# Performance work log

Measured on AMD Instinct MI355X. Metric: run time of the kernel, lower is better.

Reference implementation:

```python
import jax, jax.numpy as jnp
import numpy as np

B, N = 8192, 64
EPS = 1e-3  # diagonal jitter to guarantee strict positive-definiteness


def setup_inputs() -> dict:
    key = jax.random.key(0)
    A = jax.random.normal(key, (B, N, N), dtype=jnp.float32)
    # SPD construction: X = A A^T / N + eps*I  (eigenvalues strictly > 0)
    X = jnp.einsum('bik,bjk->bij', A, A) / N + EPS * jnp.eye(N, dtype=jnp.float32)
    return {"X": X}


def reference(X):
    # sym_logm: eig-based matrix logarithm of batched SPD matrices
    w, v = jnp.linalg.eigh(X)                    # w: [B,N], v: [B,N,N]
    logm = jnp.einsum('bik,bk,bjk->bij', v, jnp.log(w), v)  # V diag(log w) V^T
    # embed with tril=False: flatten from dim 1 -> [B, N*N]
    return logm.reshape(logm.shape[0], -1)
```

## Files before the change

### kernel.cpp

```cpp
#include <hip/hip_runtime.h>
#include <math.h>

#define NSW 12

__device__ __forceinline__ float bperm_f(int addr4, float v) {
    return __int_as_float(__builtin_amdgcn_ds_bpermute(addr4, __float_as_int(v)));
}

__global__ __launch_bounds__(128, 4) void logeig_kernel(
    const float* __restrict__ Xg, float* __restrict__ out)
{
    __shared__ __align__(16) float Wc[64 * 20];
    __shared__ float gbuf[2][2][64];
    __shared__ float nbuf[2][64];
    __shared__ float hlds[64];

    const int tid = threadIdx.x;
    const int w   = tid >> 6;
    const int l   = tid & 63;
    const int b   = blockIdx.x;

    float x[32];
    {
        const float4* __restrict__ Xb4 =
            (const float4*)(Xg + (size_t)b * 4096 + (size_t)l * 64 + 32 * w);
        #pragma unroll
        for (int q = 0; q < 8; ++q) {
            float4 v = Xb4[q];
            x[4 * q + 0] = v.x; x[4 * q + 1] = v.y;
            x[4 * q + 2] = v.z; x[4 * q + 3] = v.w;
        }
    }

    float d;
    {
        float a0 = 0.f, a1 = 0.f, a2 = 0.f, a3 = 0.f;
        #pragma unroll
        for (int k = 0; k < 32; k += 4) {
            a0 = fmaf(x[k + 0], x[k + 0], a0);
            a1 = fmaf(x[k + 1], x[k + 1], a1);
            a2 = fmaf(x[k + 2], x[k + 2], a2);
            a3 = fmaf(x[k + 3], x[k + 3], a3);
        }
        nbuf[w][l] = (a0 + a1) + (a2 + a3);
        __syncthreads();
        d = nbuf[0][l] + nbuf[1][l];
    }

    const int m  = l - 1;
    int pm = (l == 0) ? 0 : ((63 - m) % 63);
    int p0 = 0;

    for (int sweep = 0; sweep < NSW; ++sweep) {
        for (int r = 0; r < 63; ++r) {
            const int prt  = (l == 0) ? (p0 + 1)
                                      : ((pm == m) ? 0 : (pm + 1));
            const int prt4 = prt << 2;

            float xp[32];
            float a0 = 0.f, a1 = 0.f, a2 = 0.f, a3 = 0.f;
            #pragma unroll
            for (int k = 0; k < 32; k += 4) {
                xp[k + 0] = bperm_f(prt4, x[k + 0]);
                xp[k + 1] = bperm_f(prt4, x[k + 1]);
                xp[k + 2] = bperm_f(prt4, x[k + 2]);
                xp[k + 3] = bperm_f(prt4, x[k + 3]);
                a0 = fmaf(x[k + 0], xp[k + 0], a0);
                a1 = fmaf(x[k + 1], xp[k + 1], a1);
                a2 = fmaf(x[k + 2], xp[k + 2], a2);
                a3 = fmaf(x[k + 3], xp[k + 3], a3);
            }
            const float gp = (a0 + a1) + (a2 + a3);
            const float dq = bperm_f(prt4, d);

            gbuf[r & 1][w][l] = gp;
            __syncthreads();
            const float go = gbuf[r & 1][1 - w][l];
            const float g  = gp + go;

            const bool lo = l < prt;
            const bool ok = fabsf(g) > 1e-30f;

            const float num  = lo ? (dq - d) : (d - dq);
            const float zeta = num / (2.f * g);
            const float az   = fabsf(zeta);
            float tl = 1.f / (az + sqrtf(fmaf(az, az, 1.f)));
            tl = (zeta >= 0.f) ? tl : -tl;
            float tn = lo ? tl : -tl;
            tn = ok ? tn : 0.f;
            const float c = rsqrtf(fmaf(tn, tn, 1.f));
            const float s = c * tn;

            d = fmaf(-tn, g, d);

            #pragma unroll
            for (int k = 0; k < 32; ++k)
                x[k] = fmaf(-s, xp[k], c * x[k]);

            pm = (pm + 1 == 63) ? 0 : (pm + 1);
            p0 += 32; if (p0 >= 63) p0 -= 63;
        }

        float a0 = 0.f, a1 = 0.f, a2 = 0.f, a3 = 0.f;
        #pragma unroll
        for (int k = 0; k < 32; k += 4) {
            a0 = fmaf(x[k + 0], x[k + 0], a0);
            a1 = fmaf(x[k + 1], x[k + 1], a1);
            a2 = fmaf(x[k + 2], x[k + 2], a2);
            a3 = fmaf(x[k + 3], x[k + 3], a3);
        }
        __syncthreads();
        nbuf[w][l] = (a0 + a1) + (a2 + a3);
        __syncthreads();
        d = nbuf[0][l] + nbuf[1][l];
    }

    const float alpha = fmaxf(d, 1e-12f);
    const float h = 0.5f * logf(alpha) / alpha;
    if (w == 0) hlds[l] = h;

    const int cg = l >> 4;
    const int cc = l & 15;
    float* __restrict__ outb = out + (size_t)b * 4096;

    for (int rh = 0; rh < 2; ++rh) {
        float acc[16];
        #pragma unroll
        for (int k = 0; k < 16; ++k) acc[k] = 0.f;
        const int rbase = 32 * w + 16 * rh;

        for (int gi = 0; gi < 4; ++gi) {
            __syncthreads();
            if (cg == gi) {
                #pragma unroll
                for (int j = 0; j < 32; ++j) Wc[(32 * w + j) * 20 + cc] = x[j];
            }
            __syncthreads();

            #pragma unroll
            for (int hh = 0; hh < 2; ++hh) {
                float r0[8];
                #pragma unroll
                for (int j = 0; j < 8; ++j)
                    r0[j] = Wc[l * 20 + 8 * hh + j] * hlds[gi * 16 + 8 * hh + j];
                #pragma unroll
                for (int k = 0; k < 16; ++k) {
                    const int row = rbase + k;
                    const float4 wa = *(const float4*)&Wc[row * 20 + 8 * hh + 0];
                    const float4 wb = *(const float4*)&Wc[row * 20 + 8 * hh + 4];
                    acc[k] += fmaf(wa.x, r0[0], fmaf(wa.y, r0[1],
                                   fmaf(wa.z, r0[2], wa.w * r0[3])))
                            + fmaf(wb.x, r0[4], fmaf(wb.y, r0[5],
                                   fmaf(wb.z, r0[6], wb.w * r0[7])));
                }
            }
        }

        #pragma unroll
        for (int k = 0; k < 16; ++k)
            outb[(size_t)(rbase + k) * 64 + l] = acc[k];
    }
}

extern "C" void kernel_launch(void* const* d_in, const int* in_sizes, int n_in,
                              void* d_out, int out_size, void* d_ws, size_t ws_size,
                              hipStream_t stream)
{
    const float* X = (const float*)d_in[0];
    float* out = (float*)d_out;
    const int B = in_sizes[0] / 4096;
    logeig_kernel<<<dim3(B), dim3(128), 0, stream>>>(X, out);
}
```

Measured before the change: 5.117 ms.

## Pack two matrices per block and use packed float2 math in Jacobi sweeps

Each 256-thread block now processes two matrices, with each 128-thread half owning one matrix and a private shared-memory slice. The Jacobi rotation inner loops use a two-wide float vector type so the compiler can emit packed FP32 multiply/FMA instructions. The reconstruction stage's column staging is narrowed from 16 to 8 columns per pass to fit the smaller per-matrix LDS budget, which doubles the number of staging passes. Block-wide barriers now also synchronise the two independent matrices, and the launch assumes B is even.

```diff
diff --git a/kernel.cpp b/kernel.cpp
--- a/kernel.cpp
+++ b/kernel.cpp
@@ -3,48 +3,58 @@
 
 #define NSW 12
 
+typedef float v2 __attribute__((ext_vector_type(2)));
+
 __device__ __forceinline__ float bperm_f(int addr4, float v) {
     return __int_as_float(__builtin_amdgcn_ds_bpermute(addr4, __float_as_int(v)));
 }
 
-__global__ __launch_bounds__(128, 4) void logeig_kernel(
+__global__ __launch_bounds__(256, 4) void logeig_kernel(
     const float* __restrict__ Xg, float* __restrict__ out)
 {
-    __shared__ __align__(16) float Wc[64 * 20];
-    __shared__ float gbuf[2][2][64];
-    __shared__ float nbuf[2][64];
-    __shared__ float hlds[64];
+    __shared__ __align__(16) float smem[2 * 832];
 
     const int tid = threadIdx.x;
-    const int w   = tid >> 6;
+    const int mb  = tid >> 7;
+    const int w   = (tid >> 6) & 1;
     const int l   = tid & 63;
-    const int b   = blockIdx.x;
+    float* const base = smem + mb * 832;
+    float* const gb   = base;
+    const size_t bm   = (size_t)blockIdx.x * 2 + mb;
 
-    float x[32];
+    v2 x2[16];
     {
         const float4* __restrict__ Xb4 =
-            (const float4*)(Xg + (size_t)b * 4096 + (size_t)l * 64 + 32 * w);
+            (const float4*)(Xg + bm * 4096 + (size_t)l * 64 + 32 * w);
         #pragma unroll
         for (int q = 0; q < 8; ++q) {
             float4 v = Xb4[q];
-            x[4 * q + 0] = v.x; x[4 * q + 1] = v.y;
-            x[4 * q + 2] = v.z; x[4 * q + 3] = v.w;
+            x2[2 * q + 0] = (v2){v.x, v.y};
+            x2[2 * q + 1] = (v2){v.z, v.w};
         }
     }
 
+    #define SELFDOT(res)                                              \
+        {                                                             \
+            v2 a0 = {0.f,0.f}, a1 = {0.f,0.f},                        \
+               a2 = {0.f,0.f}, a3 = {0.f,0.f};                        \
+            _Pragma("unroll")                                         \
+            for (int k = 0; k < 16; k += 4) {                         \
+                a0 += x2[k + 0] * x2[k + 0];                          \
+                a1 += x2[k + 1] * x2[k + 1];                          \
+                a2 += x2[k + 2] * x2[k + 2];                          \
+                a3 += x2[k + 3] * x2[k + 3];                          \
+            }                                                         \
+            const v2 sv = (a0 + a1) + (a2 + a3);                      \
+            res = sv.x + sv.y;                                        \
+        }
+
     float d;
     {
-        float a0 = 0.f, a1 = 0.f, a2 = 0.f, a3 = 0.f;
-        #pragma unroll
-        for (int k = 0; k < 32; k += 4) {
-            a0 = fmaf(x[k + 0], x[k + 0], a0);
-            a1 = fmaf(x[k + 1], x[k + 1], a1);
-            a2 = fmaf(x[k + 2], x[k + 2], a2);
-            a3 = fmaf(x[k + 3], x[k + 3], a3);
-        }
-        nbuf[w][l] = (a0 + a1) + (a2 + a3);
+        float p; SELFDOT(p);
+        gb[w * 64 + l] = p;
         __syncthreads();
-        d = nbuf[0][l] + nbuf[1][l];
+        d = gb[l] + gb[64 + l];
     }
 
     const int m  = l - 1;
@@ -57,25 +67,30 @@
                                       : ((pm == m) ? 0 : (pm + 1));
             const int prt4 = prt << 2;
 
-            float xp[32];
-            float a0 = 0.f, a1 = 0.f, a2 = 0.f, a3 = 0.f;
+            v2 xp2[16];
+            v2 a0 = {0.f,0.f}, a1 = {0.f,0.f}, a2 = {0.f,0.f}, a3 = {0.f,0.f};
             #pragma unroll
-            for (int k = 0; k < 32; k += 4) {
-                xp[k + 0] = bperm_f(prt4, x[k + 0]);
-                xp[k + 1] = bperm_f(prt4, x[k + 1]);
-                xp[k + 2] = bperm_f(prt4, x[k + 2]);
-                xp[k + 3] = bperm_f(prt4, x[k + 3]);
-                a0 = fmaf(x[k + 0], xp[k + 0], a0);
-                a1 = fmaf(x[k + 1], xp[k + 1], a1);
-                a2 = fmaf(x[k + 2], xp[k + 2], a2);
-                a3 = fmaf(x[k + 3], xp[k + 3], a3);
+            for (int k = 0; k < 16; k += 4) {
+                xp2[k+0].x = bperm_f(prt4, x2[k+0].x);
+                xp2[k+0].y = bperm_f(prt4, x2[k+0].y);
+                xp2[k+1].x = bperm_f(prt4, x2[k+1].x);
+                xp2[k+1].y = bperm_f(prt4, x2[k+1].y);
+                xp2[k+2].x = bperm_f(prt4, x2[k+2].x);
+                xp2[k+2].y = bperm_f(prt4, x2[k+2].y);
+                xp2[k+3].x = bperm_f(prt4, x2[k+3].x);
+                xp2[k+3].y = bperm_f(prt4, x2[k+3].y);
+                a0 += x2[k + 0] * xp2[k + 0];
+                a1 += x2[k + 1] * xp2[k + 1];
+                a2 += x2[k + 2] * xp2[k + 2];
+                a3 += x2[k + 3] * xp2[k + 3];
             }
-            const float gp = (a0 + a1) + (a2 + a3);
+            const v2 sv = (a0 + a1) + (a2 + a3);
+            const float gp = sv.x + sv.y;
             const float dq = bperm_f(prt4, d);
 
-            gbuf[r & 1][w][l] = gp;
+            gb[(r & 1) * 128 + w * 64 + l] = gp;
             __syncthreads();
-            const float go = gbuf[r & 1][1 - w][l];
+            const float go = gb[(r & 1) * 128 + (1 - w) * 64 + l];
             const float g  = gp + go;
 
             const bool lo = l < prt;
@@ -94,34 +109,30 @@
             d = fmaf(-tn, g, d);
 
             #pragma unroll
-            for (int k = 0; k < 32; ++k)
-                x[k] = fmaf(-s, xp[k], c * x[k]);
+            for (int k = 0; k < 16; ++k)
+                x2[k] = c * x2[k] - s * xp2[k];
 
             pm = (pm + 1 == 63) ? 0 : (pm + 1);
             p0 += 32; if (p0 >= 63) p0 -= 63;
         }
 
-        float a0 = 0.f, a1 = 0.f, a2 = 0.f, a3 = 0.f;
-        #pragma unroll
-        for (int k = 0; k < 32; k += 4) {
-            a0 = fmaf(x[k + 0], x[k + 0], a0);
-            a1 = fmaf(x[k + 1], x[k + 1], a1);
-            a2 = fmaf(x[k + 2], x[k + 2], a2);
-            a3 = fmaf(x[k + 3], x[k + 3], a3);
-        }
+        float p; SELFDOT(p);
         __syncthreads();
-        nbuf[w][l] = (a0 + a1) + (a2 + a3);
+        gb[w * 64 + l] = p;
         __syncthreads();
-        d = nbuf[0][l] + nbuf[1][l];
+        d = gb[l] + gb[64 + l];
     }
+    #undef SELFDOT
 
     const float alpha = fmaxf(d, 1e-12f);
     const float h = 0.5f * logf(alpha) / alpha;
-    if (w == 0) hlds[l] = h;
+    float* const Wc = base;
+    float* const hl = base + 768;
+    if (w == 0) hl[l] = h;
 
-    const int cg = l >> 4;
-    const int cc = l & 15;
-    float* __restrict__ outb = out + (size_t)b * 4096;
+    const int cg = l >> 3;
+    const int cc = l & 7;
+    float* __restrict__ outb = out + bm * 4096;
 
     for (int rh = 0; rh < 2; ++rh) {
         float acc[16];
@@ -129,30 +140,31 @@
         for (int k = 0; k < 16; ++k) acc[k] = 0.f;
         const int rbase = 32 * w + 16 * rh;
 
-        for (int gi = 0; gi < 4; ++gi) {
+        for (int gi = 0; gi < 8; ++gi) {
             __syncthreads();
             if (cg == gi) {
                 #pragma unroll
-                for (int j = 0; j < 32; ++j) Wc[(32 * w + j) * 20 + cc] = x[j];
+                for (int k = 0; k < 16; ++k) {
+                    Wc[(32 * w + 2 * k + 0) * 12 + cc] = x2[k].x;
+                    Wc[(32 * w + 2 * k + 1) * 12 + cc] = x2[k].y;
+                }
             }
             __syncthreads();
 
+            float r0[8];
             #pragma unroll
-            for (int hh = 0; hh < 2; ++hh) {
-                float r0[8];
-                #pragma unroll
-                for (int j = 0; j < 8; ++j)
-                    r0[j] = Wc[l * 20 + 8 * hh + j] * hlds[gi * 16 + 8 * hh + j];
-                #pragma unroll
-                for (int k = 0; k < 16; ++k) {
-                    const int row = rbase + k;
-                    const float4 wa = *(const float4*)&Wc[row * 20 + 8 * hh + 0];
-                    const float4 wb = *(const float4*)&Wc[row * 20 + 8 * hh + 4];
-                    acc[k] += fmaf(wa.x, r0[0], fmaf(wa.y, r0[1],
-                                   fmaf(wa.z, r0[2], wa.w * r0[3])))
-                            + fmaf(wb.x, r0[4], fmaf(wb.y, r0[5],
-                                   fmaf(wb.z, r0[6], wb.w * r0[7])));
-                }
+            for (int j = 0; j < 8; ++j)
+                r0[j] = Wc[l * 12 + j] * hl[gi * 8 + j];
+
+            #pragma unroll
+            for (int k = 0; k < 16; ++k) {
+                const int row = rbase + k;
+                const float4 wa = *(const float4*)&Wc[row * 12 + 0];
+                const float4 wb = *(const float4*)&Wc[row * 12 + 4];
+                acc[k] += fmaf(wa.x, r0[0], fmaf(wa.y, r0[1],
+                               fmaf(wa.z, r0[2], wa.w * r0[3])))
+                        + fmaf(wb.x, r0[4], fmaf(wb.y, r0[5],
+                               fmaf(wb.z, r0[6], wb.w * r0[7])));
             }
         }
 
@@ -169,5 +181,5 @@
     const float* X = (const float*)d_in[0];
     float* out = (float*)d_out;
     const int B = in_sizes[0] / 4096;
-    logeig_kernel<<<dim3(B), dim3(128), 0, stream>>>(X, out);
+    logeig_kernel<<<dim3(B / 2), dim3(256), 0, stream>>>(X, out);
 }
```

Measured after the change: 5.270 ms. 3.0% more time.
